# Kernel tuning notes

Hardware: AMD Instinct MI355X
Metric: run time of the kernel (lower is better)

The kernel has to match this reference:

```python
import jax, jax.numpy as jnp
import numpy as np
from jax import lax

B, T, EPROJS, DUNITS, ATT_DIM = 32, 2048, 1024, 1024, 512
ACONV_CHANS, ACONV_FILTS = 32, 15
SCALING = 2.0


def setup_inputs() -> dict:
    key = jax.random.key(0)
    ks = jax.random.split(key, 12)
    enc_hs_pad = jax.random.normal(ks[0], (B, T, EPROJS), dtype=jnp.float32)
    enc_hs_len = jax.random.randint(ks[1], (B,), T // 2, T + 1, dtype=jnp.int32)
    dec_z = jax.random.normal(ks[2], (B, DUNITS), dtype=jnp.float32)
    ap = jax.random.uniform(ks[3], (B, T), dtype=jnp.float32)
    att_prev = ap / jnp.sum(ap, axis=1, keepdims=True)  # previous attention distribution
    # parameters (PyTorch Linear: y = x @ W^T + b; stored here pre-transposed as [in, out])
    s_enc = 1.0 / np.sqrt(EPROJS)
    s_dec = 1.0 / np.sqrt(DUNITS)
    s_att = 1.0 / np.sqrt(ACONV_CHANS)
    s_g = 1.0 / np.sqrt(ATT_DIM)
    K = 2 * ACONV_FILTS + 1
    s_c = 1.0 / np.sqrt(K)
    W_enc = jax.random.uniform(ks[4], (EPROJS, ATT_DIM), jnp.float32, -s_enc, s_enc)
    b_enc = jax.random.uniform(ks[5], (ATT_DIM,), jnp.float32, -s_enc, s_enc)
    W_dec = jax.random.uniform(ks[6], (DUNITS, ATT_DIM), jnp.float32, -s_dec, s_dec)
    W_att = jax.random.uniform(ks[7], (ACONV_CHANS, ATT_DIM), jnp.float32, -s_att, s_att)
    conv_w = jax.random.uniform(ks[8], (ACONV_CHANS, 1, K), jnp.float32, -s_c, s_c)
    W_g = jax.random.uniform(ks[9], (ATT_DIM, 1), jnp.float32, -s_g, s_g)
    b_g = jax.random.uniform(ks[10], (1,), jnp.float32, -s_g, s_g)
    return {"enc_hs_pad": enc_hs_pad, "enc_hs_len": enc_hs_len, "dec_z": dec_z,
            "att_prev": att_prev, "W_enc": W_enc, "b_enc": b_enc, "W_dec": W_dec,
            "W_att": W_att, "conv_w": conv_w, "W_g": W_g, "b_g": b_g}


def reference(enc_hs_pad, enc_hs_len, dec_z, att_prev,
              W_enc, b_enc, W_dec, W_att, conv_w, W_g, b_g):
    # pre-computed encoder projection: (B, T, A)
    pre_enc = jnp.einsum('btd,da->bta', enc_hs_pad, W_enc) + b_enc
    # location conv over previous attention: (B, 1, T) -> (B, C, T), SAME padding
    pad = (conv_w.shape[-1] - 1) // 2
    att_conv = lax.conv_general_dilated(
        att_prev[:, None, :], conv_w, window_strides=(1,),
        padding=[(pad, pad)], dimension_numbers=('NCH', 'OIH', 'NCH'))
    att_c = jnp.einsum('bct,ca->bta', att_conv, W_att)       # (B, T, A)
    dec_t = (dec_z @ W_dec)[:, None, :]                       # (B, 1, A)
    # energies: (B, T)
    e = jnp.einsum('bta,ao->bt', jnp.tanh(att_c + pre_enc + dec_t), W_g) + b_g[0]
    # pad mask: True where t >= length
    mask = jnp.arange(e.shape[1])[None, :] >= enc_hs_len[:, None]
    e = jnp.where(mask, -jnp.inf, e)
    w = jax.nn.softmax(SCALING * e, axis=1)                   # (B, T)
    c = jnp.einsum('btd,bt->bd', enc_hs_pad, w)               # (B, EPROJS)
    return c, w
```

## Files before the change

kernel.cpp:

```cpp
#include <hip/hip_runtime.h>
#include <stdint.h>

#define T_LEN 2048
#define KAUG  1056
#define M_TOT 65536
#define TILE_U16 135168

typedef __attribute__((ext_vector_type(8))) short short8;
typedef __attribute__((ext_vector_type(4))) float f32x4;
typedef unsigned int u32;
typedef unsigned short u16;

__device__ __forceinline__ u16 bf16_rn(float f){
  u32 u = __builtin_bit_cast(u32, f);
  u32 r = u + 0x7fffu + ((u >> 16) & 1u);
  return (u16)(r >> 16);
}
__device__ __forceinline__ u32 pack_rn(float lo, float hi){
  return (u32)bf16_rn(lo) | ((u32)bf16_rn(hi) << 16);
}
__device__ __forceinline__ u32 pack_trunc(float lo, float hi){
  u32 a = __builtin_bit_cast(u32, lo);
  u32 b = __builtin_bit_cast(u32, hi);
  return (a >> 16) | (b & 0xffff0000u);
}
__device__ __forceinline__ void lds_load16(const void* g, void* l){
  __builtin_amdgcn_global_load_lds(
      (const __attribute__((address_space(1))) u32*)g,
      (__attribute__((address_space(3))) u32*)l, 16, 0, 0);
}

__global__ void k_build_bt(const float* __restrict__ W_enc,
                           const float* __restrict__ W_att,
                           u16* __restrict__ Bt){
  __shared__ float tile[32][33];
  int k0 = blockIdx.x * 32, n0 = blockIdx.y * 32;
  int tx = threadIdx.x & 31, ty = threadIdx.x >> 5;
  #pragma unroll
  for (int i = 0; i < 4; i++){
    int k = k0 + i*8 + ty;
    int n = n0 + tx;
    float v = (k < 1024) ? W_enc[k*512 + n] : W_att[(k-1024)*512 + n];
    tile[i*8+ty][tx] = v;
  }
  __syncthreads();
  #pragma unroll
  for (int i = 0; i < 4; i++){
    int n = n0 + i*8 + ty;
    int k = k0 + tx;
    Bt[(size_t)n*KAUG + k] = bf16_rn(tile[tx][i*8+ty]);
  }
}

__global__ void k_bias(const float* __restrict__ dec_z,
                       const float* __restrict__ W_dec,
                       const float* __restrict__ b_enc,
                       float* __restrict__ bias){
  __shared__ float red[4][64];
  int b = blockIdx.y, n0 = blockIdx.x * 64;
  int nl = threadIdx.x & 63, ks = threadIdx.x >> 6;
  int n = n0 + nl;
  const float* dz = dec_z + b*1024;
  float s = 0.f;
  #pragma unroll 4
  for (int k = ks*256; k < ks*256 + 256; k++) s += dz[k] * W_dec[k*512 + n];
  red[ks][nl] = s;
  __syncthreads();
  if (threadIdx.x < 64){
    int nn = n0 + threadIdx.x;
    bias[b*512 + nn] = b_enc[nn] + red[0][threadIdx.x] + red[1][threadIdx.x]
                     + red[2][threadIdx.x] + red[3][threadIdx.x];
  }
}

__global__ void k_pack(const float* __restrict__ enc, u16* __restrict__ Apack){
  int e = blockIdx.x*256 + threadIdx.x;
  int row   = e >> 7;
  int chunk = e & 127;
  const float* src = enc + (size_t)row*1024 + chunk*8;
  f32x4 a = *(const f32x4*)src;
  f32x4 b = *(const f32x4*)(src + 4);
  union { u32 u[4]; short8 v; } cv;
  cv.u[0] = pack_rn(a.x, a.y);
  cv.u[1] = pack_rn(a.z, a.w);
  cv.u[2] = pack_rn(b.x, b.y);
  cv.u[3] = pack_rn(b.z, b.w);
  int mblk = row >> 7, t = chunk >> 2, kin = (chunk & 3)*8;
  u16* d = Apack + (size_t)mblk*TILE_U16 + t*4096 + (row & 127)*32 + kin;
  *(short8*)d = cv.v;
}

__global__ void k_conv_p(const float* __restrict__ att_prev,
                         const float* __restrict__ conv_w,
                         u16* __restrict__ Apack){
  int idx = blockIdx.x*256 + threadIdx.x;
  int c = idx & 31;
  int bt = idx >> 5;
  int b = bt >> 11, t = bt & 2047;
  const float* ap = att_prev + b*2048;
  const float* cw = conv_w + c*31;
  float s = 0.f;
  #pragma unroll
  for (int j = 0; j < 31; j++){
    int tt = t + j - 15;
    float a = (tt >= 0 && tt < 2048) ? ap[tt] : 0.f;
    s += cw[j] * a;
  }
  int mblk = bt >> 7;
  Apack[(size_t)mblk*TILE_U16 + 32*4096 + (bt & 127)*32 + c] = bf16_rn(s);
}

__launch_bounds__(256, 4)
__global__ void k_gemm_energy_p(const u16* __restrict__ Apack,
                                const u16* __restrict__ Bt,
                                const float* __restrict__ bias,
                                const float* __restrict__ Wg,
                                float* __restrict__ ePart){
  __shared__ __align__(16) u16 Ash[3][4096];
  __shared__ float eRed[2][128];

  const int tid  = threadIdx.x;
  const int lane = tid & 63;
  const int wid  = tid >> 6;
  const int wave_m = wid >> 1, wave_n = wid & 1;
  const int bidx = blockIdx.x;
  const int xcd  = bidx & 7;
  const int s_sq = bidx >> 3;
  const int nblk = s_sq & 3;
  const int mblk = ((s_sq >> 2) << 3) + xcd;
  const int row0 = mblk << 7;
  const int b    = mblk >> 4;

  f32x4 acc[4][4];
  #pragma unroll
  for (int i = 0; i < 4; i++)
    #pragma unroll
    for (int j = 0; j < 4; j++) acc[i][j] = (f32x4)(0.f);

  const int fr_m = lane & 15;
  const int kg   = lane >> 4;

  const u16* Atile = Apack + (size_t)mblk*TILE_U16;
  const u16* asrc  = Atile + (wid*2)*512 + lane*8;
  const u16* BtN   = Bt + (size_t)(nblk*128)*KAUG;

  const u16* bptr0 = BtN + (size_t)(wave_n*64 +  0 + fr_m)*KAUG + kg*8;
  const u16* bptr1 = BtN + (size_t)(wave_n*64 + 16 + fr_m)*KAUG + kg*8;
  const u16* bptr2 = BtN + (size_t)(wave_n*64 + 32 + fr_m)*KAUG + kg*8;
  const u16* bptr3 = BtN + (size_t)(wave_n*64 + 48 + fr_m)*KAUG + kg*8;

  int aroff[4];
  #pragma unroll
  for (int mi = 0; mi < 4; mi++){
    int m = wave_m*64 + mi*16 + fr_m;
    aroff[mi] = m*32 + kg*8;
  }

  auto STAGE = [&](int t, int bufi){
    const u16* s0 = asrc + t*4096;
    lds_load16(s0,       &Ash[bufi][(wid*2 + 0)*512]);
    lds_load16(s0 + 512, &Ash[bufi][(wid*2 + 1)*512]);
  };
  auto LOADBF = [&](int t, short8* bf){
    bf[0] = *(const short8*)(bptr0 + t*32);
    bf[1] = *(const short8*)(bptr1 + t*32);
    bf[2] = *(const short8*)(bptr2 + t*32);
    bf[3] = *(const short8*)(bptr3 + t*32);
  };
  auto COMPUTE = [&](int bufi, const short8* bf){
    #pragma unroll
    for (int mi = 0; mi < 4; mi++){
      short8 af = *(const short8*)&Ash[bufi][aroff[mi]];
      #pragma unroll
      for (int ni = 0; ni < 4; ni++)
        acc[mi][ni] = __builtin_amdgcn_mfma_f32_16x16x32_bf16(af, bf[ni], acc[mi][ni], 0, 0, 0);
    }
  };

  short8 bfA[4], bfB[4];
  STAGE(0, 0);
  LOADBF(0, bfA);
  STAGE(1, 1);

  int bE = 0;
  #pragma unroll 1
  for (int i = 0; i < 16; i++){
    int t  = 2*i;
    int bO = (bE == 2) ? 0 : bE + 1;
    int sE = (bO == 2) ? 0 : bO + 1;
    int sO = bE;
    LOADBF(t+1, bfB);
    asm volatile("s_waitcnt vmcnt(6)" ::: "memory");
    __builtin_amdgcn_s_barrier();
    asm volatile("" ::: "memory");
    if (t < 31) STAGE(t+2, sE);
    COMPUTE(bE, bfA);
    LOADBF(t+2, bfA);
    asm volatile("s_waitcnt vmcnt(6)" ::: "memory");
    __builtin_amdgcn_s_barrier();
    asm volatile("" ::: "memory");
    if (t+1 < 31) STAGE(t+3, sO);
    COMPUTE(bO, bfB);
    bE = sE;
  }
  asm volatile("s_waitcnt vmcnt(0)" ::: "memory");
  __builtin_amdgcn_s_barrier();
  asm volatile("" ::: "memory");
  COMPUTE(bE, bfA);

  float wg[4], bs[4];
  #pragma unroll
  for (int ni = 0; ni < 4; ni++){
    int ng = nblk*128 + wave_n*64 + ni*16 + fr_m;
    wg[ni] = Wg[ng];
    bs[ni] = bias[b*512 + ng];
  }
  #pragma unroll
  for (int mi = 0; mi < 4; mi++){
    #pragma unroll
    for (int reg = 0; reg < 4; reg++){
      float s = 0.f;
      #pragma unroll
      for (int ni = 0; ni < 4; ni++){
        float v  = acc[mi][ni][reg] + bs[ni];
        float e2 = __expf(2.f * v);
        float th = 1.f - 2.f/(e2 + 1.f);
        s += wg[ni] * th;
      }
      s += __shfl_xor(s, 1);
      s += __shfl_xor(s, 2);
      s += __shfl_xor(s, 4);
      s += __shfl_xor(s, 8);
      if (fr_m == 0){
        int rowl = wave_m*64 + mi*16 + kg*4 + reg;
        eRed[wave_n][rowl] = s;
      }
    }
  }
  __syncthreads();
  if (tid < 128)
    ePart[(size_t)nblk*M_TOT + row0 + tid] = eRed[0][tid] + eRed[1][tid];
}

__global__ void k_conv_f(const float* __restrict__ att_prev,
                         const float* __restrict__ conv_w,
                         float* __restrict__ attT){
  int idx = blockIdx.x*256 + threadIdx.x;
  int c = idx & 31;
  int bt = idx >> 5;
  int b = bt >> 11, t = bt & 2047;
  const float* ap = att_prev + b*2048;
  const float* cw = conv_w + c*31;
  float s = 0.f;
  #pragma unroll
  for (int j = 0; j < 31; j++){
    int tt = t + j - 15;
    float a = (tt >= 0 && tt < 2048) ? ap[tt] : 0.f;
    s += cw[j] * a;
  }
  attT[(size_t)bt*32 + c] = s;
}

__launch_bounds__(256, 3)
__global__ void k_gemm_energy_f(const float* __restrict__ enc,
                                const float* __restrict__ attT,
                                const u16* __restrict__ Bt,
                                const float* __restrict__ bias,
                                const float* __restrict__ Wg,
                                float* __restrict__ ePart){
  __shared__ __align__(16) u16 Ash[2][128*32];
  __shared__ float eRed[2][128];
  const int tid  = threadIdx.x;
  const int lane = tid & 63;
  const int wid  = tid >> 6;
  const int wave_m = wid >> 1, wave_n = wid & 1;
  const int bidx = blockIdx.x;
  const int xcd  = bidx & 7;
  const int s_sq = bidx >> 3;
  const int nblk = s_sq & 3;
  const int mblk = ((s_sq >> 2) << 3) + xcd;
  const int row0 = mblk << 7;
  const int b    = mblk >> 4;
  f32x4 acc[4][4];
  #pragma unroll
  for (int i = 0; i < 4; i++)
    #pragma unroll
    for (int j = 0; j < 4; j++) acc[i][j] = (f32x4)(0.f);
  const int srow = lane >> 2;
  const int sc   = lane & 3;
  const int fr_m = lane & 15;
  const int kg   = lane >> 4;
  const u16* BtN = Bt + (size_t)(nblk*128)*KAUG;
  int r0q[2], ldsoff[2];
  #pragma unroll
  for (int q = 0; q < 2; q++){
    int r = wid*32 + q*16 + srow;
    r0q[q] = r;
    ldsoff[q] = r*32 + (sc ^ ((r >> 1) & 3))*8;
  }
  int aroff[4];
  #pragma unroll
  for (int mi = 0; mi < 4; mi++){
    int m = wave_m*64 + mi*16 + fr_m;
    aroff[mi] = m*32 + (kg ^ ((m >> 1) & 3))*8;
  }
  int bnrow[4];
  #pragma unroll
  for (int ni = 0; ni < 4; ni++)
    bnrow[ni] = wave_n*64 + ni*16 + fr_m;
  auto LOADA = [&](int t, f32x4* ra){
    const float* base; size_t rstr;
    if (t < 32){ base = enc + (size_t)row0*1024 + t*32; rstr = 1024; }
    else       { base = attT + (size_t)row0*32;         rstr = 32;  }
    #pragma unroll
    for (int q = 0; q < 2; q++){
      const float* p = base + (size_t)r0q[q]*rstr + sc*8;
      ra[q*2+0] = *(const f32x4*)(p);
      ra[q*2+1] = *(const f32x4*)(p + 4);
    }
  };
  auto LOADBF = [&](int t, short8* bf){
    #pragma unroll
    for (int ni = 0; ni < 4; ni++)
      bf[ni] = *(const short8*)(BtN + (size_t)bnrow[ni]*KAUG + t*32 + kg*8);
  };
  auto WRITEA = [&](const f32x4* ra, int bi){
    #pragma unroll
    for (int q = 0; q < 2; q++){
      f32x4 lo = ra[q*2+0], hi = ra[q*2+1];
      union { u32 u[4]; short8 v; } cv;
      cv.u[0] = pack_trunc(lo.x, lo.y);
      cv.u[1] = pack_trunc(lo.z, lo.w);
      cv.u[2] = pack_trunc(hi.x, hi.y);
      cv.u[3] = pack_trunc(hi.z, hi.w);
      *(short8*)&Ash[bi][ldsoff[q]] = cv.v;
    }
  };
  auto COMPUTE = [&](int bi, const short8* bf){
    const u16* Ab = &Ash[bi][0];
    #pragma unroll
    for (int mi = 0; mi < 4; mi++){
      short8 af = *(const short8*)(Ab + aroff[mi]);
      #pragma unroll
      for (int ni = 0; ni < 4; ni++)
        acc[mi][ni] = __builtin_amdgcn_mfma_f32_16x16x32_bf16(af, bf[ni], acc[mi][ni], 0, 0, 0);
    }
  };
  f32x4 raA[4], raB[4];
  short8 bfA[4], bfB[4];
  LOADA(0, raA); LOADBF(0, bfA);
  #pragma unroll 1
  for (int i = 0; i < 16; i++){
    int kk = 2*i;
    LOADA(kk+1, raB); LOADBF(kk+1, bfB);
    WRITEA(raA, 0);
    asm volatile("s_waitcnt lgkmcnt(0)" ::: "memory");
    __builtin_amdgcn_s_barrier();
    asm volatile("" ::: "memory");
    COMPUTE(0, bfA);
    LOADA(kk+2, raA); LOADBF(kk+2, bfA);
    WRITEA(raB, 1);
    asm volatile("s_waitcnt lgkmcnt(0)" ::: "memory");
    __builtin_amdgcn_s_barrier();
    asm volatile("" ::: "memory");
    COMPUTE(1, bfB);
  }
  WRITEA(raA, 0);
  asm volatile("s_waitcnt lgkmcnt(0)" ::: "memory");
  __builtin_amdgcn_s_barrier();
  asm volatile("" ::: "memory");
  COMPUTE(0, bfA);
  float wg[4], bs[4];
  #pragma unroll
  for (int ni = 0; ni < 4; ni++){
    int ng = nblk*128 + wave_n*64 + ni*16 + fr_m;
    wg[ni] = Wg[ng];
    bs[ni] = bias[b*512 + ng];
  }
  #pragma unroll
  for (int mi = 0; mi < 4; mi++){
    #pragma unroll
    for (int reg = 0; reg < 4; reg++){
      float s = 0.f;
      #pragma unroll
      for (int ni = 0; ni < 4; ni++){
        float v  = acc[mi][ni][reg] + bs[ni];
        float e2 = __expf(2.f * v);
        float th = 1.f - 2.f/(e2 + 1.f);
        s += wg[ni] * th;
      }
      s += __shfl_xor(s, 1);
      s += __shfl_xor(s, 2);
      s += __shfl_xor(s, 4);
      s += __shfl_xor(s, 8);
      if (fr_m == 0){
        int rowl = wave_m*64 + mi*16 + kg*4 + reg;
        eRed[wave_n][rowl] = s;
      }
    }
  }
  __syncthreads();
  if (tid < 128)
    ePart[(size_t)nblk*M_TOT + row0 + tid] = eRed[0][tid] + eRed[1][tid];
}

__global__ void k_softmax(const float* __restrict__ ePart,
                          const int* __restrict__ lens,
                          float* __restrict__ wout){
  int b = blockIdx.x, tid = threadIdx.x;
  int lane = tid & 63, wid = tid >> 6;
  int len = lens[b];
  __shared__ float red[4];
  float x[8]; float m = -3.0e38f;
  #pragma unroll
  for (int i = 0; i < 8; i++){
    int t = tid + i*256;
    int idx = b*2048 + t;
    float e = ePart[idx] + ePart[M_TOT + idx] + ePart[2*M_TOT + idx] + ePart[3*M_TOT + idx];
    float xx = (t < len) ? 2.0f*e : -3.0e38f;
    x[i] = xx; m = fmaxf(m, xx);
  }
  #pragma unroll
  for (int o = 1; o < 64; o <<= 1) m = fmaxf(m, __shfl_xor(m, o));
  if (lane == 0) red[wid] = m;
  __syncthreads();
  m = fmaxf(fmaxf(red[0], red[1]), fmaxf(red[2], red[3]));
  float s = 0.f;
  #pragma unroll
  for (int i = 0; i < 8; i++){
    float ex = (x[i] > -1.0e38f) ? __expf(x[i] - m) : 0.f;
    x[i] = ex; s += ex;
  }
  #pragma unroll
  for (int o = 1; o < 64; o <<= 1) s += __shfl_xor(s, o);
  __syncthreads();
  if (lane == 0) red[wid] = s;
  __syncthreads();
  s = red[0] + red[1] + red[2] + red[3];
  float inv = 1.0f / s;
  #pragma unroll
  for (int i = 0; i < 8; i++){
    int t = tid + i*256;
    wout[b*2048 + t] = x[i]*inv;
  }
}

__global__ void k_ctx_partial(const float* __restrict__ enc,
                              const float* __restrict__ w,
                              float* __restrict__ cPart){
  int dc = blockIdx.x, tc = blockIdx.y, b = blockIdx.z;
  int d = dc*256 + threadIdx.x;
  const float* ep = enc + ((size_t)(b*2048 + tc*256))*1024 + d;
  const float* wp = w + b*2048 + tc*256;
  float s0 = 0, s1 = 0, s2 = 0, s3 = 0;
  #pragma unroll 2
  for (int t = 0; t < 256; t += 4){
    s0 += wp[t+0] * ep[(size_t)(t+0)*1024];
    s1 += wp[t+1] * ep[(size_t)(t+1)*1024];
    s2 += wp[t+2] * ep[(size_t)(t+2)*1024];
    s3 += wp[t+3] * ep[(size_t)(t+3)*1024];
  }
  cPart[((size_t)tc*32 + b)*1024 + d] = (s0 + s1) + (s2 + s3);
}

__global__ void k_ctx_reduce(const float* __restrict__ cPart, float* __restrict__ cOut){
  int idx = blockIdx.x*256 + threadIdx.x;
  float s = 0.f;
  #pragma unroll
  for (int tc = 0; tc < 8; tc++) s += cPart[tc*32768 + idx];
  cOut[idx] = s;
}

extern "C" void kernel_launch(void* const* d_in, const int* in_sizes, int n_in,
                              void* d_out, int out_size, void* d_ws, size_t ws_size,
                              hipStream_t stream){
  (void)in_sizes; (void)n_in; (void)out_size;
  const float* enc    = (const float*)d_in[0];
  const int*   lens   = (const int*)  d_in[1];
  const float* dec_z  = (const float*)d_in[2];
  const float* att_p  = (const float*)d_in[3];
  const float* W_enc  = (const float*)d_in[4];
  const float* b_enc  = (const float*)d_in[5];
  const float* W_dec  = (const float*)d_in[6];
  const float* W_att  = (const float*)d_in[7];
  const float* conv_w = (const float*)d_in[8];
  const float* W_g    = (const float*)d_in[9];

  float* c_out = (float*)d_out;
  float* w_out = c_out + 32*1024;

  char* ws = (char*)d_ws;

  if (ws_size >= 141656064ull){
    u16*   Bt    = (u16*)  (ws);
    float* bias  = (float*)(ws + 1081344);
    float* ePart = (float*)(ws + 1146880);
    float* cPart = (float*)(ws + 2195456);
    u16*   Apack = (u16*)  (ws + 3244032);

    hipLaunchKernelGGL(k_build_bt,      dim3(33,16),  dim3(256), 0, stream, W_enc, W_att, Bt);
    hipLaunchKernelGGL(k_bias,          dim3(8,32),   dim3(256), 0, stream, dec_z, W_dec, b_enc, bias);
    hipLaunchKernelGGL(k_pack,          dim3(32768),  dim3(256), 0, stream, enc, Apack);
    hipLaunchKernelGGL(k_conv_p,        dim3(8192),   dim3(256), 0, stream, att_p, conv_w, Apack);
    hipLaunchKernelGGL(k_gemm_energy_p, dim3(2048),   dim3(256), 0, stream, Apack, Bt, bias, W_g, ePart);
    hipLaunchKernelGGL(k_softmax,       dim3(32),     dim3(256), 0, stream, ePart, lens, w_out);
    hipLaunchKernelGGL(k_ctx_partial,   dim3(4,8,32), dim3(256), 0, stream, enc, w_out, cPart);
    hipLaunchKernelGGL(k_ctx_reduce,    dim3(128),    dim3(256), 0, stream, cPart, c_out);
  } else {
    u16*   Bt    = (u16*)  (ws);
    float* attT  = (float*)(ws + 1081344);
    float* bias  = (float*)(ws + 1081344 + 8388608);
    float* ePart = (float*)(ws + 1081344 + 8388608 + 65536);
    float* cPart = (float*)(ws + 1081344 + 8388608 + 65536 + 1048576);

    hipLaunchKernelGGL(k_build_bt,      dim3(33,16),  dim3(256), 0, stream, W_enc, W_att, Bt);
    hipLaunchKernelGGL(k_bias,          dim3(8,32),   dim3(256), 0, stream, dec_z, W_dec, b_enc, bias);
    hipLaunchKernelGGL(k_conv_f,        dim3(8192),   dim3(256), 0, stream, att_p, conv_w, attT);
    hipLaunchKernelGGL(k_gemm_energy_f, dim3(2048),   dim3(256), 0, stream, enc, attT, Bt, bias, W_g, ePart);
    hipLaunchKernelGGL(k_softmax,       dim3(32),     dim3(256), 0, stream, ePart, lens, w_out);
    hipLaunchKernelGGL(k_ctx_partial,   dim3(4,8,32), dim3(256), 0, stream, enc, w_out, cPart);
    hipLaunchKernelGGL(k_ctx_reduce,    dim3(128),    dim3(256), 0, stream, cPart, c_out);
  }
}
```

Before: 634.4 us.

## Double GEMM K-step to 64 with zero-padded K and larger LDS stages

The packed-A energy GEMM now processes a K-chunk of 64 per pipeline stage instead of 32. The augmented K dimension is zero-padded from 1056 to 1088 in both the weight matrix and the packed activations, so the loop runs 8 double-iterations instead of 16, with half as many barriers. The LDS buffers double in size, occupancy bounds drop from 4 to 3 blocks, and s_setprio is raised around the MFMA blocks. The cost is extra zero-padding work and a larger workspace.

```diff
diff --git a/kernel.cpp b/kernel.cpp
--- a/kernel.cpp
+++ b/kernel.cpp
@@ -3,8 +3,9 @@
 
 #define T_LEN 2048
 #define KAUG  1056
+#define KAUG2 1088
 #define M_TOT 65536
-#define TILE_U16 135168
+#define TILE_U16 139264
 
 typedef __attribute__((ext_vector_type(8))) short short8;
 typedef __attribute__((ext_vector_type(4))) float f32x4;
@@ -32,7 +33,7 @@
 
 __global__ void k_build_bt(const float* __restrict__ W_enc,
                            const float* __restrict__ W_att,
-                           u16* __restrict__ Bt){
+                           u16* __restrict__ Bt, int stride){
   __shared__ float tile[32][33];
   int k0 = blockIdx.x * 32, n0 = blockIdx.y * 32;
   int tx = threadIdx.x & 31, ty = threadIdx.x >> 5;
@@ -40,7 +41,8 @@
   for (int i = 0; i < 4; i++){
     int k = k0 + i*8 + ty;
     int n = n0 + tx;
-    float v = (k < 1024) ? W_enc[k*512 + n] : W_att[(k-1024)*512 + n];
+    float v = (k < 1024) ? W_enc[k*512 + n]
+            : (k < 1056) ? W_att[(k-1024)*512 + n] : 0.f;
     tile[i*8+ty][tx] = v;
   }
   __syncthreads();
@@ -48,7 +50,7 @@
   for (int i = 0; i < 4; i++){
     int n = n0 + i*8 + ty;
     int k = k0 + tx;
-    Bt[(size_t)n*KAUG + k] = bf16_rn(tile[tx][i*8+ty]);
+    Bt[(size_t)n*stride + k] = bf16_rn(tile[tx][i*8+ty]);
   }
 }
 
@@ -107,16 +109,18 @@
     s += cw[j] * a;
   }
   int mblk = bt >> 7;
-  Apack[(size_t)mblk*TILE_U16 + 32*4096 + (bt & 127)*32 + c] = bf16_rn(s);
-}
-
-__launch_bounds__(256, 4)
+  u16* base = Apack + (size_t)mblk*TILE_U16 + (bt & 127)*32 + c;
+  base[32*4096] = bf16_rn(s);
+  base[33*4096] = 0;
+}
+
+__launch_bounds__(256, 3)
 __global__ void k_gemm_energy_p(const u16* __restrict__ Apack,
                                 const u16* __restrict__ Bt,
                                 const float* __restrict__ bias,
                                 const float* __restrict__ Wg,
                                 float* __restrict__ ePart){
-  __shared__ __align__(16) u16 Ash[3][4096];
+  __shared__ __align__(16) u16 Ash[3][8192];
   __shared__ float eRed[2][128];
 
   const int tid  = threadIdx.x;
@@ -141,13 +145,13 @@
   const int kg   = lane >> 4;
 
   const u16* Atile = Apack + (size_t)mblk*TILE_U16;
-  const u16* asrc  = Atile + (wid*2)*512 + lane*8;
-  const u16* BtN   = Bt + (size_t)(nblk*128)*KAUG;
-
-  const u16* bptr0 = BtN + (size_t)(wave_n*64 +  0 + fr_m)*KAUG + kg*8;
-  const u16* bptr1 = BtN + (size_t)(wave_n*64 + 16 + fr_m)*KAUG + kg*8;
-  const u16* bptr2 = BtN + (size_t)(wave_n*64 + 32 + fr_m)*KAUG + kg*8;
-  const u16* bptr3 = BtN + (size_t)(wave_n*64 + 48 + fr_m)*KAUG + kg*8;
+  const u16* asrc  = Atile + wid*2048 + lane*8;
+  const u16* BtN   = Bt + (size_t)(nblk*128)*KAUG2;
+
+  const u16* bptr0 = BtN + (size_t)(wave_n*64 +  0 + fr_m)*KAUG2 + kg*8;
+  const u16* bptr1 = BtN + (size_t)(wave_n*64 + 16 + fr_m)*KAUG2 + kg*8;
+  const u16* bptr2 = BtN + (size_t)(wave_n*64 + 32 + fr_m)*KAUG2 + kg*8;
+  const u16* bptr3 = BtN + (size_t)(wave_n*64 + 48 + fr_m)*KAUG2 + kg*8;
 
   int aroff[4];
   #pragma unroll
@@ -156,57 +160,68 @@
     aroff[mi] = m*32 + kg*8;
   }
 
-  auto STAGE = [&](int t, int bufi){
-    const u16* s0 = asrc + t*4096;
-    lds_load16(s0,       &Ash[bufi][(wid*2 + 0)*512]);
-    lds_load16(s0 + 512, &Ash[bufi][(wid*2 + 1)*512]);
-  };
-  auto LOADBF = [&](int t, short8* bf){
-    bf[0] = *(const short8*)(bptr0 + t*32);
-    bf[1] = *(const short8*)(bptr1 + t*32);
-    bf[2] = *(const short8*)(bptr2 + t*32);
-    bf[3] = *(const short8*)(bptr3 + t*32);
-  };
-  auto COMPUTE = [&](int bufi, const short8* bf){
-    #pragma unroll
-    for (int mi = 0; mi < 4; mi++){
-      short8 af = *(const short8*)&Ash[bufi][aroff[mi]];
+  auto STAGE2 = [&](int ph, int bufi){
+    const u16* s0 = asrc + ph*8192;
+    #pragma unroll
+    for (int q = 0; q < 4; q++)
+      lds_load16(s0 + q*512, &Ash[bufi][(wid*4 + q)*512]);
+  };
+  auto LOADBF2 = [&](int ph, short8* bf){
+    int o = ph*64;
+    bf[0] = *(const short8*)(bptr0 + o);
+    bf[1] = *(const short8*)(bptr1 + o);
+    bf[2] = *(const short8*)(bptr2 + o);
+    bf[3] = *(const short8*)(bptr3 + o);
+    bf[4] = *(const short8*)(bptr0 + o + 32);
+    bf[5] = *(const short8*)(bptr1 + o + 32);
+    bf[6] = *(const short8*)(bptr2 + o + 32);
+    bf[7] = *(const short8*)(bptr3 + o + 32);
+  };
+  auto COMPUTE2 = [&](int bufi, const short8* bf){
+    __builtin_amdgcn_s_setprio(1);
+    #pragma unroll
+    for (int sub = 0; sub < 2; sub++){
       #pragma unroll
-      for (int ni = 0; ni < 4; ni++)
-        acc[mi][ni] = __builtin_amdgcn_mfma_f32_16x16x32_bf16(af, bf[ni], acc[mi][ni], 0, 0, 0);
+      for (int mi = 0; mi < 4; mi++){
+        short8 af = *(const short8*)&Ash[bufi][sub*4096 + aroff[mi]];
+        #pragma unroll
+        for (int ni = 0; ni < 4; ni++)
+          acc[mi][ni] = __builtin_amdgcn_mfma_f32_16x16x32_bf16(af, bf[sub*4+ni], acc[mi][ni], 0, 0, 0);
+      }
     }
-  };
-
-  short8 bfA[4], bfB[4];
-  STAGE(0, 0);
-  LOADBF(0, bfA);
-  STAGE(1, 1);
+    __builtin_amdgcn_s_setprio(0);
+  };
+
+  short8 bfA[8], bfB[8];
+  STAGE2(0, 0);
+  LOADBF2(0, bfA);
+  STAGE2(1, 1);
 
   int bE = 0;
   #pragma unroll 1
-  for (int i = 0; i < 16; i++){
-    int t  = 2*i;
+  for (int i = 0; i < 8; i++){
+    int p  = 2*i;
     int bO = (bE == 2) ? 0 : bE + 1;
     int sE = (bO == 2) ? 0 : bO + 1;
     int sO = bE;
-    LOADBF(t+1, bfB);
-    asm volatile("s_waitcnt vmcnt(6)" ::: "memory");
+    LOADBF2(p+1, bfB);
+    asm volatile("s_waitcnt vmcnt(12)" ::: "memory");
     __builtin_amdgcn_s_barrier();
     asm volatile("" ::: "memory");
-    if (t < 31) STAGE(t+2, sE);
-    COMPUTE(bE, bfA);
-    LOADBF(t+2, bfA);
-    asm volatile("s_waitcnt vmcnt(6)" ::: "memory");
+    STAGE2(p+2, sE);
+    COMPUTE2(bE, bfA);
+    LOADBF2(p+2, bfA);
+    asm volatile("s_waitcnt vmcnt(12)" ::: "memory");
     __builtin_amdgcn_s_barrier();
     asm volatile("" ::: "memory");
-    if (t+1 < 31) STAGE(t+3, sO);
-    COMPUTE(bO, bfB);
+    if (i < 7) STAGE2(p+3, sO);
+    COMPUTE2(bO, bfB);
     bE = sE;
   }
   asm volatile("s_waitcnt vmcnt(0)" ::: "memory");
   __builtin_amdgcn_s_barrier();
   asm volatile("" ::: "memory");
-  COMPUTE(bE, bfA);
+  COMPUTE2(bE, bfA);
 
   float wg[4], bs[4];
   #pragma unroll
@@ -491,14 +506,14 @@
 
   char* ws = (char*)d_ws;
 
-  if (ws_size >= 141656064ull){
+  if (ws_size >= 145883136ull){
     u16*   Bt    = (u16*)  (ws);
-    float* bias  = (float*)(ws + 1081344);
-    float* ePart = (float*)(ws + 1146880);
-    float* cPart = (float*)(ws + 2195456);
-    u16*   Apack = (u16*)  (ws + 3244032);
-
-    hipLaunchKernelGGL(k_build_bt,      dim3(33,16),  dim3(256), 0, stream, W_enc, W_att, Bt);
+    float* bias  = (float*)(ws + 1114112);
+    float* ePart = (float*)(ws + 1179648);
+    float* cPart = (float*)(ws + 2228224);
+    u16*   Apack = (u16*)  (ws + 3276800);
+
+    hipLaunchKernelGGL(k_build_bt,      dim3(34,16),  dim3(256), 0, stream, W_enc, W_att, Bt, KAUG2);
     hipLaunchKernelGGL(k_bias,          dim3(8,32),   dim3(256), 0, stream, dec_z, W_dec, b_enc, bias);
     hipLaunchKernelGGL(k_pack,          dim3(32768),  dim3(256), 0, stream, enc, Apack);
     hipLaunchKernelGGL(k_conv_p,        dim3(8192),   dim3(256), 0, stream, att_p, conv_w, Apack);
@@ -513,7 +528,7 @@
     float* ePart = (float*)(ws + 1081344 + 8388608 + 65536);
     float* cPart = (float*)(ws + 1081344 + 8388608 + 65536 + 1048576);
 
-    hipLaunchKernelGGL(k_build_bt,      dim3(33,16),  dim3(256), 0, stream, W_enc, W_att, Bt);
+    hipLaunchKernelGGL(k_build_bt,      dim3(33,16),  dim3(256), 0, stream, W_enc, W_att, Bt, KAUG);
     hipLaunchKernelGGL(k_bias,          dim3(8,32),   dim3(256), 0, stream, dec_z, W_dec, b_enc, bias);
     hipLaunchKernelGGL(k_conv_f,        dim3(8192),   dim3(256), 0, stream, att_p, conv_w, attT);
     hipLaunchKernelGGL(k_gemm_energy_f, dim3(2048),   dim3(256), 0, stream, enc, attT, Bt, bias, W_g, ePart);
```

Result: slower. 682.1 us (+7.5%).
